# Optimization experiments

Hardware: AMD Instinct MI355X
Metric: run time of the kernel (lower is better)

Reference implementation:

```python
import jax, jax.numpy as jnp
import numpy as np

ALPHA = 1.8   # Levy stability index (undefined global in source; chosen heavy-tailed)
BETA = 0.0    # symmetric
SIGMA = 0.5
DEPTH = 25
DIM = 64
HID = 100
BATCH = 262144


def _levy_noise(u_raw, w_raw):
    """Chambers-Mallows-Stuck sampler for symmetric alpha-stable (beta=0).
    u_raw, w_raw ~ U(0,1); returns clipped noise, scale=0.1, clamp [-10,10]."""
    U = jnp.pi * (u_raw - 0.5)                       # U(-pi/2, pi/2)
    W = -jnp.log(jnp.clip(w_raw, 1e-12, 1.0))        # Exp(1)
    inv_a = 1.0 / ALPHA
    X = (jnp.sin(ALPHA * U) / jnp.cos(U) ** inv_a) * \
        (jnp.cos(U - ALPHA * U) / jnp.clip(W, 1e-12, None)) ** ((1.0 - ALPHA) * inv_a)
    return jnp.clip(0.1 * X, -10.0, 10.0)


def setup_inputs() -> dict:
    key = jax.random.key(0)
    ks = jax.random.split(key, 8)
    d, h = DIM, HID
    return {
        "x": jax.random.normal(ks[0], (BATCH, d), dtype=jnp.float32),
        "u_raw": jax.random.uniform(ks[1], (DEPTH, d), dtype=jnp.float32),
        "w_raw": jax.random.uniform(ks[2], (DEPTH, d), dtype=jnp.float32),
        "W_down": jax.random.normal(ks[3], (d, d), dtype=jnp.float32) / np.sqrt(d),
        "b_down": jnp.zeros((d,), jnp.float32),
        "W_drift": jax.random.normal(ks[4], (d, d), dtype=jnp.float32) / np.sqrt(d),
        "b_drift": jnp.zeros((d,), jnp.float32),
        "W1": jax.random.normal(ks[5], (d, h), dtype=jnp.float32) / np.sqrt(d),
        "b1": jnp.zeros((h,), jnp.float32),
        "W2": jax.random.normal(ks[6], (h, 1), dtype=jnp.float32) / np.sqrt(h),
        "b2": jnp.zeros((1,), jnp.float32),
    }


def reference(x, u_raw, w_raw, W_down, b_down, W_drift, b_drift, W1, b1, W2, b2):
    dt = 1.0 / DEPTH
    out = x @ W_down + b_down                                   # [B, d]
    # diffusion logit on the INITIAL state, held fixed through the loop
    logit = jax.nn.relu(out @ W1 + b1) @ W2 + b2                # [B, 1]
    scale = SIGMA * jax.nn.sigmoid(logit) * dt ** (1.0 / ALPHA)  # [B, 1]
    noise = _levy_noise(u_raw, w_raw)                           # [DEPTH, d]

    def step(out, n):
        drift = jax.nn.relu(out @ W_drift + b_drift) + out      # DriftNet: relu(lin)+x
        return out + drift * dt + scale * n, None

    out, _ = jax.lax.scan(step, out, noise)
    drift_out = jax.nn.relu(out @ W_drift + b_drift) + out
    return drift_out, out
```

## Files before the change

kernel.cpp:

```cpp
#include <hip/hip_runtime.h>

#define DEPTH 25
#define DIM   64
#define HID   100

typedef _Float16 f16x4 __attribute__((ext_vector_type(4)));
typedef _Float16 f16x8 __attribute__((ext_vector_type(8)));
typedef __fp16   h2    __attribute__((ext_vector_type(2)));
typedef float    f32x4 __attribute__((ext_vector_type(4)));
typedef float    f32x2 __attribute__((ext_vector_type(2)));

__global__ __launch_bounds__(64) void levy_noise_kernel(
    const float* __restrict__ u_raw, const float* __restrict__ w_raw,
    float* __restrict__ noise)
{
    const int idx = blockIdx.x * 64 + threadIdx.x;
    if (idx >= DEPTH * DIM) return;
    float u = u_raw[idx];
    float w = w_raw[idx];
    float U  = 3.14159265358979323846f * (u - 0.5f);
    float Wv = -logf(fminf(fmaxf(w, 1e-12f), 1.0f));
    float t1 = sinf(1.8f * U) / powf(cosf(U), 0.5555555555555556f);
    float ratio = cosf(0.8f * U) / fmaxf(Wv, 1e-12f);
    float X = t1 * powf(ratio, -0.4444444444444444f);
    noise[idx] = fminf(fmaxf(0.1f * X, -10.0f), 10.0f);
}

union frag_u { h2 p[4]; f16x8 v; };

__global__ __launch_bounds__(256) void sdenet_fused(
    const float* __restrict__ x,      const float* __restrict__ noise_g,
    const float* __restrict__ W_down, const float* __restrict__ b_down,
    const float* __restrict__ W_drift,const float* __restrict__ b_drift,
    const float* __restrict__ W1,     const float* __restrict__ b1,
    const float* __restrict__ W2,     const float* __restrict__ b2,
    float* __restrict__ out, int batch)
{
    __shared__ float    noise_lds[DEPTH * DIM];
    __shared__ _Float16 wbuf[8192];

    const int tid  = threadIdx.x;
    const int wave = tid >> 6;
    const int lane = tid & 63;
    const int r    = lane & 15;
    const int g    = lane >> 4;
    const int row  = blockIdx.x * 64 + wave * 16 + r;
    const int fbase = lane * 8;
    const float dt = 0.04f;

    {
        const float4* src = (const float4*)noise_g;
        float4* dst = (float4*)noise_lds;
        for (int idx = tid; idx < DEPTH * DIM / 4; idx += 256)
            dst[idx] = src[idx];
    }
    for (int idx2 = tid; idx2 < 2048; idx2 += 256) {
        const int fi    = idx2 >> 8;
        const int lane2 = (idx2 >> 2) & 63;
        const int j     = (idx2 & 3) * 2;
        const int m     = (fi >> 1) * 16 + (lane2 & 15);
        const int k     = (fi & 1) * 32 + ((j & 4) ? 16 : 0)
                        + (lane2 >> 4) * 4 + (j & 3);
        *(h2*)(wbuf + idx2 * 2) =
            __builtin_amdgcn_cvt_pkrtz(W_down[k * DIM + m],
                                       W_down[(k + 1) * DIM + m]);
        *(h2*)(wbuf + 4096 + idx2 * 2) =
            __builtin_amdgcn_cvt_pkrtz(dt * W_drift[k * DIM + m],
                                       dt * W_drift[(k + 1) * DIM + m]);
    }

    float4 xlo[2], xhi[2];
    #pragma unroll
    for (int kt = 0; kt < 2; ++kt) {
        xlo[kt] = *(const float4*)(x + row * DIM + kt * 32 + g * 4);
        xhi[kt] = *(const float4*)(x + row * DIM + kt * 32 + 16 + g * 4);
    }
    __syncthreads();

    f16x8 bfrag[2];
    #pragma unroll
    for (int kt = 0; kt < 2; ++kt) {
        frag_u u;
        u.p[0] = __builtin_amdgcn_cvt_pkrtz(xlo[kt].x, xlo[kt].y);
        u.p[1] = __builtin_amdgcn_cvt_pkrtz(xlo[kt].z, xlo[kt].w);
        u.p[2] = __builtin_amdgcn_cvt_pkrtz(xhi[kt].x, xhi[kt].y);
        u.p[3] = __builtin_amdgcn_cvt_pkrtz(xhi[kt].z, xhi[kt].w);
        bfrag[kt] = u.v;
    }

    f32x2 out2[4][2];
    #pragma unroll
    for (int Mt = 0; Mt < 4; ++Mt) {
        f32x4 acc = *(const f32x4*)(b_down + Mt * 16 + g * 4);
        #pragma unroll
        for (int kt = 0; kt < 2; ++kt)
            acc = __builtin_amdgcn_mfma_f32_16x16x32_f16(
                *(const f16x8*)(wbuf + (Mt * 2 + kt) * 512 + fbase),
                bfrag[kt], acc, 0, 0, 0);
        out2[Mt][0][0] = acc[0]; out2[Mt][0][1] = acc[1];
        out2[Mt][1][0] = acc[2]; out2[Mt][1][1] = acc[3];
    }

    auto refresh = [&]() {
        #pragma unroll
        for (int kt = 0; kt < 2; ++kt) {
            frag_u u;
            u.p[0] = __builtin_amdgcn_cvt_pkrtz(out2[2*kt  ][0][0], out2[2*kt  ][0][1]);
            u.p[1] = __builtin_amdgcn_cvt_pkrtz(out2[2*kt  ][1][0], out2[2*kt  ][1][1]);
            u.p[2] = __builtin_amdgcn_cvt_pkrtz(out2[2*kt+1][0][0], out2[2*kt+1][0][1]);
            u.p[3] = __builtin_amdgcn_cvt_pkrtz(out2[2*kt+1][1][0], out2[2*kt+1][1][1]);
            bfrag[kt] = u.v;
        }
    };
    refresh();

    f16x8 aWd[4][2];
    #pragma unroll
    for (int Mt = 0; Mt < 4; ++Mt)
        #pragma unroll
        for (int kt = 0; kt < 2; ++kt)
            aWd[Mt][kt] = *(const f16x8*)(wbuf + 4096 + (Mt * 2 + kt) * 512 + fbase);

    f32x4 biasd[4];
    #pragma unroll
    for (int Mt = 0; Mt < 4; ++Mt) {
        f32x4 b = *(const f32x4*)(b_drift + Mt * 16 + g * 4);
        biasd[Mt][0] = b[0] * dt; biasd[Mt][1] = b[1] * dt;
        biasd[Mt][2] = b[2] * dt; biasd[Mt][3] = b[3] * dt;
    }

    __syncthreads();

    for (int idx2 = tid; idx2 < 3584; idx2 += 256) {
        const int fi    = idx2 >> 8;
        const int lane2 = (idx2 >> 2) & 63;
        const int j     = (idx2 & 3) * 2;
        const int n     = (fi >> 1) * 16 + (lane2 & 15);
        const int k     = (fi & 1) * 32 + ((j & 4) ? 16 : 0)
                        + (lane2 >> 4) * 4 + (j & 3);
        const float v0 = (n < HID) ? W1[k * HID + n] : 0.0f;
        const float v1 = (n < HID) ? W1[(k + 1) * HID + n] : 0.0f;
        *(h2*)(wbuf + idx2 * 2) = __builtin_amdgcn_cvt_pkrtz(v0, v1);
    }
    __syncthreads();

    float partial = 0.0f;
    #pragma unroll
    for (int Mt = 0; Mt < 7; ++Mt) {
        f32x4 acc;
        #pragma unroll
        for (int reg = 0; reg < 4; ++reg) {
            const int n = Mt * 16 + g * 4 + reg;
            acc[reg] = (n < HID) ? b1[n] : 0.0f;
        }
        #pragma unroll
        for (int kt = 0; kt < 2; ++kt)
            acc = __builtin_amdgcn_mfma_f32_16x16x32_f16(
                *(const f16x8*)(wbuf + (Mt * 2 + kt) * 512 + fbase),
                bfrag[kt], acc, 0, 0, 0);
        #pragma unroll
        for (int reg = 0; reg < 4; ++reg) {
            const int n = Mt * 16 + g * 4 + reg;
            if (n < HID) partial += fmaxf(acc[reg], 0.0f) * W2[n];
        }
    }
    partial += __shfl_xor(partial, 16);
    partial += __shfl_xor(partial, 32);
    const float logit = partial + b2[0];
    const float scale = 0.5f * (1.0f / (1.0f + expf(-logit)))
                      * powf(0.04f, 1.0f / 1.8f);
    const f32x2 scale2 = { scale, scale };
    const f32x2 c104   = { 1.04f, 1.04f };
    const f32x2 zero2  = { 0.0f, 0.0f };

    for (int t = 0; t < DEPTH; ++t) {
        f32x4 nz[4];
        #pragma unroll
        for (int Mt = 0; Mt < 4; ++Mt)
            nz[Mt] = *(const f32x4*)(noise_lds + t * DIM + Mt * 16 + g * 4);

        f32x4 acc[4];
        #pragma unroll
        for (int Mt = 0; Mt < 4; ++Mt) {
            acc[Mt] = __builtin_amdgcn_mfma_f32_16x16x32_f16(
                aWd[Mt][0], bfrag[0], biasd[Mt], 0, 0, 0);
            acc[Mt] = __builtin_amdgcn_mfma_f32_16x16x32_f16(
                aWd[Mt][1], bfrag[1], acc[Mt], 0, 0, 0);
        }
        #pragma unroll
        for (int Mt = 0; Mt < 4; ++Mt) {
            #pragma unroll
            for (int h = 0; h < 2; ++h) {
                f32x2 a2 = { acc[Mt][2*h], acc[Mt][2*h+1] };
                f32x2 n2 = { nz[Mt][2*h],  nz[Mt][2*h+1] };
                f32x2 rel = __builtin_elementwise_max(a2, zero2);
                f32x2 tmp = __builtin_elementwise_fma(out2[Mt][h], c104, rel);
                out2[Mt][h] = __builtin_elementwise_fma(scale2, n2, tmp);
            }
        }
        refresh();
    }

    const long long out2_off = (long long)batch * DIM;
    #pragma unroll
    for (int Mt = 0; Mt < 4; ++Mt) {
        f32x4 acc = __builtin_amdgcn_mfma_f32_16x16x32_f16(
            aWd[Mt][0], bfrag[0], biasd[Mt], 0, 0, 0);
        acc = __builtin_amdgcn_mfma_f32_16x16x32_f16(
            aWd[Mt][1], bfrag[1], acc, 0, 0, 0);
        float o0 = out2[Mt][0][0], o1 = out2[Mt][0][1];
        float o2 = out2[Mt][1][0], o3 = out2[Mt][1][1];
        float4 dv, ov;
        dv.x = fmaf(fmaxf(acc[0], 0.0f), 25.0f, o0);
        dv.y = fmaf(fmaxf(acc[1], 0.0f), 25.0f, o1);
        dv.z = fmaf(fmaxf(acc[2], 0.0f), 25.0f, o2);
        dv.w = fmaf(fmaxf(acc[3], 0.0f), 25.0f, o3);
        ov.x = o0; ov.y = o1; ov.z = o2; ov.w = o3;
        *(float4*)(out + (long long)row * DIM + Mt * 16 + g * 4) = dv;
        *(float4*)(out + out2_off + (long long)row * DIM + Mt * 16 + g * 4) = ov;
    }
}

extern "C" void kernel_launch(void* const* d_in, const int* in_sizes, int n_in,
                              void* d_out, int out_size, void* d_ws, size_t ws_size,
                              hipStream_t stream) {
    const float* x       = (const float*)d_in[0];
    const float* u_raw   = (const float*)d_in[1];
    const float* w_raw   = (const float*)d_in[2];
    const float* W_down  = (const float*)d_in[3];
    const float* b_down  = (const float*)d_in[4];
    const float* W_drift = (const float*)d_in[5];
    const float* b_drift = (const float*)d_in[6];
    const float* W1      = (const float*)d_in[7];
    const float* b1      = (const float*)d_in[8];
    const float* W2      = (const float*)d_in[9];
    const float* b2      = (const float*)d_in[10];
    float* out   = (float*)d_out;
    float* noise = (float*)d_ws;

    const int batch = in_sizes[0] / DIM;
    const int blocks = batch / 64;

    levy_noise_kernel<<<DEPTH, 64, 0, stream>>>(u_raw, w_raw, noise);
    sdenet_fused<<<blocks, 256, 0, stream>>>(
        x, noise, W_down, b_down, W_drift, b_drift,
        W1, b1, W2, b2, out, batch);
}
```

Baseline: 288.2 us.

## Split weight LDS buffers, merge syncs, move drift bias to LDS, unroll loop

Gives W_down, W_drift and W1 their own LDS buffers so all weight staging happens before a single barrier, removing two __syncthreads and the reuse of one buffer. The drift bias is kept in LDS and reloaded each step instead of being held in registers. The launch bounds now ask for 4 blocks per CU and the 25-step loop is fully unrolled. Together these aim to cut register pressure and barrier stalls and raise occupancy, at the cost of more LDS per block (about 38 KB) and extra LDS reads inside the step loop.

```diff
diff --git a/kernel.cpp b/kernel.cpp
--- a/kernel.cpp
+++ b/kernel.cpp
@@ -28,7 +28,7 @@
 
 union frag_u { h2 p[4]; f16x8 v; };
 
-__global__ __launch_bounds__(256) void sdenet_fused(
+__global__ __launch_bounds__(256, 4) void sdenet_fused(
     const float* __restrict__ x,      const float* __restrict__ noise_g,
     const float* __restrict__ W_down, const float* __restrict__ b_down,
     const float* __restrict__ W_drift,const float* __restrict__ b_drift,
@@ -37,7 +37,10 @@
     float* __restrict__ out, int batch)
 {
     __shared__ float    noise_lds[DEPTH * DIM];
-    __shared__ _Float16 wbuf[8192];
+    __shared__ float    bias_lds[DIM];
+    __shared__ _Float16 wdown[4096];
+    __shared__ _Float16 wdrift[4096];
+    __shared__ _Float16 w1buf[7168];
 
     const int tid  = threadIdx.x;
     const int wave = tid >> 6;
@@ -51,9 +54,14 @@
     {
         const float4* src = (const float4*)noise_g;
         float4* dst = (float4*)noise_lds;
-        for (int idx = tid; idx < DEPTH * DIM / 4; idx += 256)
-            dst[idx] = src[idx];
-    }
+        #pragma unroll
+        for (int it = 0; it < 2; ++it) {
+            int idx = tid + it * 256;
+            if (idx < DEPTH * DIM / 4) dst[idx] = src[idx];
+        }
+    }
+    if (tid < DIM) bias_lds[tid] = dt * b_drift[tid];
+
     for (int idx2 = tid; idx2 < 2048; idx2 += 256) {
         const int fi    = idx2 >> 8;
         const int lane2 = (idx2 >> 2) & 63;
@@ -61,76 +69,13 @@
         const int m     = (fi >> 1) * 16 + (lane2 & 15);
         const int k     = (fi & 1) * 32 + ((j & 4) ? 16 : 0)
                         + (lane2 >> 4) * 4 + (j & 3);
-        *(h2*)(wbuf + idx2 * 2) =
+        *(h2*)(wdown + idx2 * 2) =
             __builtin_amdgcn_cvt_pkrtz(W_down[k * DIM + m],
                                        W_down[(k + 1) * DIM + m]);
-        *(h2*)(wbuf + 4096 + idx2 * 2) =
+        *(h2*)(wdrift + idx2 * 2) =
             __builtin_amdgcn_cvt_pkrtz(dt * W_drift[k * DIM + m],
                                        dt * W_drift[(k + 1) * DIM + m]);
     }
-
-    float4 xlo[2], xhi[2];
-    #pragma unroll
-    for (int kt = 0; kt < 2; ++kt) {
-        xlo[kt] = *(const float4*)(x + row * DIM + kt * 32 + g * 4);
-        xhi[kt] = *(const float4*)(x + row * DIM + kt * 32 + 16 + g * 4);
-    }
-    __syncthreads();
-
-    f16x8 bfrag[2];
-    #pragma unroll
-    for (int kt = 0; kt < 2; ++kt) {
-        frag_u u;
-        u.p[0] = __builtin_amdgcn_cvt_pkrtz(xlo[kt].x, xlo[kt].y);
-        u.p[1] = __builtin_amdgcn_cvt_pkrtz(xlo[kt].z, xlo[kt].w);
-        u.p[2] = __builtin_amdgcn_cvt_pkrtz(xhi[kt].x, xhi[kt].y);
-        u.p[3] = __builtin_amdgcn_cvt_pkrtz(xhi[kt].z, xhi[kt].w);
-        bfrag[kt] = u.v;
-    }
-
-    f32x2 out2[4][2];
-    #pragma unroll
-    for (int Mt = 0; Mt < 4; ++Mt) {
-        f32x4 acc = *(const f32x4*)(b_down + Mt * 16 + g * 4);
-        #pragma unroll
-        for (int kt = 0; kt < 2; ++kt)
-            acc = __builtin_amdgcn_mfma_f32_16x16x32_f16(
-                *(const f16x8*)(wbuf + (Mt * 2 + kt) * 512 + fbase),
-                bfrag[kt], acc, 0, 0, 0);
-        out2[Mt][0][0] = acc[0]; out2[Mt][0][1] = acc[1];
-        out2[Mt][1][0] = acc[2]; out2[Mt][1][1] = acc[3];
-    }
-
-    auto refresh = [&]() {
-        #pragma unroll
-        for (int kt = 0; kt < 2; ++kt) {
-            frag_u u;
-            u.p[0] = __builtin_amdgcn_cvt_pkrtz(out2[2*kt  ][0][0], out2[2*kt  ][0][1]);
-            u.p[1] = __builtin_amdgcn_cvt_pkrtz(out2[2*kt  ][1][0], out2[2*kt  ][1][1]);
-            u.p[2] = __builtin_amdgcn_cvt_pkrtz(out2[2*kt+1][0][0], out2[2*kt+1][0][1]);
-            u.p[3] = __builtin_amdgcn_cvt_pkrtz(out2[2*kt+1][1][0], out2[2*kt+1][1][1]);
-            bfrag[kt] = u.v;
-        }
-    };
-    refresh();
-
-    f16x8 aWd[4][2];
-    #pragma unroll
-    for (int Mt = 0; Mt < 4; ++Mt)
-        #pragma unroll
-        for (int kt = 0; kt < 2; ++kt)
-            aWd[Mt][kt] = *(const f16x8*)(wbuf + 4096 + (Mt * 2 + kt) * 512 + fbase);
-
-    f32x4 biasd[4];
-    #pragma unroll
-    for (int Mt = 0; Mt < 4; ++Mt) {
-        f32x4 b = *(const f32x4*)(b_drift + Mt * 16 + g * 4);
-        biasd[Mt][0] = b[0] * dt; biasd[Mt][1] = b[1] * dt;
-        biasd[Mt][2] = b[2] * dt; biasd[Mt][3] = b[3] * dt;
-    }
-
-    __syncthreads();
-
     for (int idx2 = tid; idx2 < 3584; idx2 += 256) {
         const int fi    = idx2 >> 8;
         const int lane2 = (idx2 >> 2) & 63;
@@ -140,9 +85,53 @@
                         + (lane2 >> 4) * 4 + (j & 3);
         const float v0 = (n < HID) ? W1[k * HID + n] : 0.0f;
         const float v1 = (n < HID) ? W1[(k + 1) * HID + n] : 0.0f;
-        *(h2*)(wbuf + idx2 * 2) = __builtin_amdgcn_cvt_pkrtz(v0, v1);
+        *(h2*)(w1buf + idx2 * 2) = __builtin_amdgcn_cvt_pkrtz(v0, v1);
+    }
+
+    float4 xlo[2], xhi[2];
+    #pragma unroll
+    for (int kt = 0; kt < 2; ++kt) {
+        xlo[kt] = *(const float4*)(x + row * DIM + kt * 32 + g * 4);
+        xhi[kt] = *(const float4*)(x + row * DIM + kt * 32 + 16 + g * 4);
     }
     __syncthreads();
+
+    f16x8 bfrag[2];
+    #pragma unroll
+    for (int kt = 0; kt < 2; ++kt) {
+        frag_u u;
+        u.p[0] = __builtin_amdgcn_cvt_pkrtz(xlo[kt].x, xlo[kt].y);
+        u.p[1] = __builtin_amdgcn_cvt_pkrtz(xlo[kt].z, xlo[kt].w);
+        u.p[2] = __builtin_amdgcn_cvt_pkrtz(xhi[kt].x, xhi[kt].y);
+        u.p[3] = __builtin_amdgcn_cvt_pkrtz(xhi[kt].z, xhi[kt].w);
+        bfrag[kt] = u.v;
+    }
+
+    f32x2 out2[4][2];
+    #pragma unroll
+    for (int Mt = 0; Mt < 4; ++Mt) {
+        f32x4 acc = *(const f32x4*)(b_down + Mt * 16 + g * 4);
+        #pragma unroll
+        for (int kt = 0; kt < 2; ++kt)
+            acc = __builtin_amdgcn_mfma_f32_16x16x32_f16(
+                *(const f16x8*)(wdown + (Mt * 2 + kt) * 512 + fbase),
+                bfrag[kt], acc, 0, 0, 0);
+        out2[Mt][0][0] = acc[0]; out2[Mt][0][1] = acc[1];
+        out2[Mt][1][0] = acc[2]; out2[Mt][1][1] = acc[3];
+    }
+
+    auto refresh = [&]() {
+        #pragma unroll
+        for (int kt = 0; kt < 2; ++kt) {
+            frag_u u;
+            u.p[0] = __builtin_amdgcn_cvt_pkrtz(out2[2*kt  ][0][0], out2[2*kt  ][0][1]);
+            u.p[1] = __builtin_amdgcn_cvt_pkrtz(out2[2*kt  ][1][0], out2[2*kt  ][1][1]);
+            u.p[2] = __builtin_amdgcn_cvt_pkrtz(out2[2*kt+1][0][0], out2[2*kt+1][0][1]);
+            u.p[3] = __builtin_amdgcn_cvt_pkrtz(out2[2*kt+1][1][0], out2[2*kt+1][1][1]);
+            bfrag[kt] = u.v;
+        }
+    };
+    refresh();
 
     float partial = 0.0f;
     #pragma unroll
@@ -156,7 +145,7 @@
         #pragma unroll
         for (int kt = 0; kt < 2; ++kt)
             acc = __builtin_amdgcn_mfma_f32_16x16x32_f16(
-                *(const f16x8*)(wbuf + (Mt * 2 + kt) * 512 + fbase),
+                *(const f16x8*)(w1buf + (Mt * 2 + kt) * 512 + fbase),
                 bfrag[kt], acc, 0, 0, 0);
         #pragma unroll
         for (int reg = 0; reg < 4; ++reg) {
@@ -173,6 +162,14 @@
     const f32x2 c104   = { 1.04f, 1.04f };
     const f32x2 zero2  = { 0.0f, 0.0f };
 
+    f16x8 aWd[4][2];
+    #pragma unroll
+    for (int Mt = 0; Mt < 4; ++Mt)
+        #pragma unroll
+        for (int kt = 0; kt < 2; ++kt)
+            aWd[Mt][kt] = *(const f16x8*)(wdrift + (Mt * 2 + kt) * 512 + fbase);
+
+    #pragma unroll
     for (int t = 0; t < DEPTH; ++t) {
         f32x4 nz[4];
         #pragma unroll
@@ -182,8 +179,9 @@
         f32x4 acc[4];
         #pragma unroll
         for (int Mt = 0; Mt < 4; ++Mt) {
+            acc[Mt] = *(const f32x4*)(bias_lds + Mt * 16 + g * 4);
             acc[Mt] = __builtin_amdgcn_mfma_f32_16x16x32_f16(
-                aWd[Mt][0], bfrag[0], biasd[Mt], 0, 0, 0);
+                aWd[Mt][0], bfrag[0], acc[Mt], 0, 0, 0);
             acc[Mt] = __builtin_amdgcn_mfma_f32_16x16x32_f16(
                 aWd[Mt][1], bfrag[1], acc[Mt], 0, 0, 0);
         }
@@ -204,8 +202,9 @@
     const long long out2_off = (long long)batch * DIM;
     #pragma unroll
     for (int Mt = 0; Mt < 4; ++Mt) {
-        f32x4 acc = __builtin_amdgcn_mfma_f32_16x16x32_f16(
-            aWd[Mt][0], bfrag[0], biasd[Mt], 0, 0, 0);
+        f32x4 acc = *(const f32x4*)(bias_lds + Mt * 16 + g * 4);
+        acc = __builtin_amdgcn_mfma_f32_16x16x32_f16(
+            aWd[Mt][0], bfrag[0], acc, 0, 0, 0);
         acc = __builtin_amdgcn_mfma_f32_16x16x32_f16(
             aWd[Mt][1], bfrag[1], acc, 0, 0, 0);
         float o0 = out2[Mt][0][0], o1 = out2[Mt][0][1];
```

After: 269.5 us. -6.5%, faster.
